# Kernel tuning notes

Measured on AMD Instinct MI355X. Metric: run time of the kernel, lower is better.

## Reference

```python
import jax, jax.numpy as jnp
import numpy as np

INPUT_DIM = 1024
UNITS = 1024

def setup_inputs() -> dict:
    key = jax.random.key(0)
    ks = jax.random.split(key, 7)
    B, S = 4, 2048
    x = jax.random.normal(ks[0], (B, S, INPUT_DIM), dtype=jnp.float32)
    # nn.Linear weights stored as [out, in]; biases [out]
    scale = 1.0 / np.sqrt(INPUT_DIM)
    Wq = jax.random.uniform(ks[1], (UNITS, INPUT_DIM), jnp.float32, -scale, scale)
    bq = jax.random.uniform(ks[2], (UNITS,), jnp.float32, -scale, scale)
    Wk = jax.random.uniform(ks[3], (UNITS, INPUT_DIM), jnp.float32, -scale, scale)
    bk = jax.random.uniform(ks[4], (UNITS,), jnp.float32, -scale, scale)
    Wv = jax.random.uniform(ks[5], (UNITS, INPUT_DIM), jnp.float32, -scale, scale)
    bv = jax.random.uniform(ks[6], (UNITS,), jnp.float32, -scale, scale)
    return {"x": x, "Wq": Wq, "bq": bq, "Wk": Wk, "bk": bk, "Wv": Wv, "bv": bv}

def reference(x, Wq, bq, Wk, bk, Wv, bv):
    # Q/K/V projections: [B,S,D] @ [D,U]
    Q = jnp.einsum('bsd,ud->bsu', x, Wq) + bq
    K = jnp.einsum('bsd,ud->bsu', x, Wk) + bk
    V = jnp.einsum('bsd,ud->bsu', x, Wv) + bv
    scores = jnp.einsum('bqu,bku->bqk', Q, K) / jnp.sqrt(jnp.float32(UNITS))
    attn = jax.nn.softmax(scores, axis=-1)
    return jnp.einsum('bqk,bku->bqu', attn, V)
```

## Files before the change

### kernel.cpp

```cpp
#include <hip/hip_runtime.h>
#include <cstdint>
#include <cstddef>


typedef unsigned short ushort_t;
typedef __attribute__((ext_vector_type(8))) short short8;
typedef __attribute__((ext_vector_type(4))) float f32x4;

#define AS1 __attribute__((address_space(1)))
#define AS3 __attribute__((address_space(3)))

__device__ __forceinline__ ushort_t f2bf(float f) {
    unsigned int u = __float_as_uint(f);
    u += 0x7FFFu + ((u >> 16) & 1u);
    return (ushort_t)(u >> 16);
}
__device__ __forceinline__ float bf2f(ushort_t b) {
    return __uint_as_float(((unsigned)b) << 16);
}

__device__ __forceinline__ void async_ld16(const void* g, unsigned lds_off) {
    __builtin_amdgcn_global_load_lds((const AS1 void*)(uintptr_t)g,
                                     (AS3 void*)(uintptr_t)lds_off,
                                     16, 0, 0);
}

template <typename OT, int EPI, int NB, int BK, int CX, int CY>
__global__ __launch_bounds__(256, 2) void gemm_bt(
    const ushort_t* __restrict__ A, const ushort_t* __restrict__ B0,
    const ushort_t* __restrict__ B1,
    const float* __restrict__ bias0, const float* __restrict__ bias1,
    OT* __restrict__ C0, OT* __restrict__ C1,
    int K, int lda, int ldb, int ldc, float scale,
    long long aOffZ, long long bOffZ, long long cOffZ)
{
    constexpr int P     = BK / 8;
    constexpr int NCALL = BK / 16;
    constexpr int RPC   = 2048 / BK;

    __shared__ __align__(16) ushort_t As[128 * BK];
    __shared__ __align__(16) ushort_t Bs[NB][128 * BK];
    __shared__ float rs[128];

    const int tid  = threadIdx.x;
    const int wave = tid >> 6;
    const int lane = tid & 63;

    const int GX  = gridDim.x, GY = gridDim.y, GZ = gridDim.z;
    const int bid = blockIdx.x + GX * (blockIdx.y + GY * blockIdx.z);
    const int xcd = bid & 7;
    const int jj  = bid >> 3;
    const int CZ  = (GX * GY * GZ) / (8 * CX * CY);
    const int NCX = GX / CX, NCY = GY / CY;
    const int cx  = xcd % NCX;
    const int ct  = xcd / NCX;
    const int cy  = ct % NCY, cz = ct / NCY;
    const int bx  = cx * CX + (jj % CX);
    const int by  = cy * CY + ((jj / CX) % CY);
    const int bz  = cz * CZ + jj / (CX * CY);

    A  += (size_t)bz * aOffZ;
    B0 += (size_t)bz * bOffZ;
    if (NB == 2) B1 += (size_t)bz * bOffZ;

    const int m0 = by * 128;
    const int n0 = bx * 128;
    const int wm = (wave >> 1) * 64;
    const int wn = (wave & 1) * 64;

    const unsigned ldsA  = (unsigned)(uintptr_t)&As[0];
    const unsigned ldsB0 = (unsigned)(uintptr_t)&Bs[0][0];
    const unsigned ldsB1 = (NB == 2) ? (unsigned)(uintptr_t)&Bs[NB - 1][0] : 0;

    const int srow = wave * (RPC / 4) + lane / P;
    const int cd   = ((lane & (P - 1)) - srow) & (P - 1);
    const ushort_t* gA  = A  + (size_t)(m0 + srow) * lda + cd * 8;
    const ushort_t* gB0 = B0 + (size_t)(n0 + srow) * ldb + cd * 8;
    const ushort_t* gB1 = (NB == 2) ? B1 + (size_t)(n0 + srow) * ldb + cd * 8
                                    : nullptr;
    const unsigned lw = (wave << 10);

    const int frow = lane & 15;
    const int fg   = lane >> 4;

    f32x4 acc[NB][4][4] = {};
    float rsacc[4] = {0.f, 0.f, 0.f, 0.f};

    for (int k0 = 0; k0 < K; k0 += BK) {
        if (k0) __syncthreads();
#pragma unroll
        for (int c = 0; c < NCALL; ++c) {
            const size_t ro = (size_t)c * RPC;
            async_ld16(gA + ro * lda, ldsA + c * 4096 + lw);
            async_ld16(gB0 + ro * ldb, ldsB0 + c * 4096 + lw);
            if (NB == 2) async_ld16(gB1 + ro * ldb, ldsB1 + c * 4096 + lw);
        }
        gA += BK; gB0 += BK; if (NB == 2) gB1 += BK;
        __syncthreads();

#pragma unroll
        for (int t = 0; t < BK / 32; ++t) {
            const int pa = (((t << 2) + fg + frow) & (P - 1)) << 3;
            short8 af[4], bf[4];
#pragma unroll
            for (int i = 0; i < 4; ++i)
                af[i] = *(const short8*)&As[(wm + i * 16 + frow) * BK + pa];
            if (EPI == 4 && wn == 0) {
#pragma unroll
                for (int i = 0; i < 4; ++i)
#pragma unroll
                    for (int e = 0; e < 8; ++e)
                        rsacc[i] += bf2f((ushort_t)af[i][e]);
            }
#pragma unroll
            for (int j = 0; j < 4; ++j)
                bf[j] = *(const short8*)&Bs[0][(wn + j * 16 + frow) * BK + pa];
#pragma unroll
            for (int i = 0; i < 4; ++i)
#pragma unroll
                for (int j = 0; j < 4; ++j)
                    acc[0][i][j] = __builtin_amdgcn_mfma_f32_16x16x32_bf16(
                        af[i], bf[j], acc[0][i][j], 0, 0, 0);
            if (NB == 2) {
#pragma unroll
                for (int j = 0; j < 4; ++j)
                    bf[j] = *(const short8*)&Bs[NB - 1][(wn + j * 16 + frow) * BK + pa];
#pragma unroll
                for (int i = 0; i < 4; ++i)
#pragma unroll
                    for (int j = 0; j < 4; ++j)
                        acc[NB - 1][i][j] = __builtin_amdgcn_mfma_f32_16x16x32_bf16(
                            af[i], bf[j], acc[NB - 1][i][j], 0, 0, 0);
            }
        }
    }

    if (EPI == 4) {
        if (wn == 0) {
#pragma unroll
            for (int i = 0; i < 4; ++i) {
                float s = rsacc[i];
                s += __shfl_xor(s, 16, 64);
                s += __shfl_xor(s, 32, 64);
                rs[wm + i * 16 + frow] = s;
            }
        }
        __syncthreads();
    }

    const int r0 = (lane >> 4) << 2;
    const int c0 = lane & 15;
#pragma unroll
    for (int o = 0; o < NB; ++o) {
        OT* C = (o == 0) ? C0 : C1;
        C += (size_t)bz * cOffZ;
        const float* bia = (o == 0) ? bias0 : bias1;
#pragma unroll
        for (int i = 0; i < 4; ++i) {
            float bm[4];
            if (EPI == 2) {
#pragma unroll
                for (int r = 0; r < 4; ++r)
                    bm[r] = bias0[m0 + wm + i * 16 + r0 + r];
            }
            if (EPI == 4) {
#pragma unroll
                for (int r = 0; r < 4; ++r)
                    bm[r] = 1.0f / rs[wm + i * 16 + r0 + r];
            }
#pragma unroll
            for (int j = 0; j < 4; ++j) {
                const int n = n0 + wn + j * 16 + c0;
                const float bn = (EPI == 1) ? bia[n] : 0.f;
#pragma unroll
                for (int r = 0; r < 4; ++r) {
                    const int m = m0 + wm + i * 16 + r0 + r;
                    float v = acc[o][i][j][r] * scale;
                    if (EPI == 1) v += bn;
                    if (EPI == 2) v += bm[r];
                    if (EPI == 3) v = __expf(v);
                    if (EPI == 4) v *= bm[r];
                    if constexpr (sizeof(OT) == 2)
                        C[(size_t)m * ldc + n] = f2bf(v);
                    else
                        C[(size_t)m * ldc + n] = v;
                }
            }
        }
    }
}

__global__ __launch_bounds__(256) void cvt_all(
    const float* __restrict__ x,  const float* __restrict__ wq,
    const float* __restrict__ wk, const float* __restrict__ wv,
    ushort_t* __restrict__ xb,  ushort_t* __restrict__ wqb,
    ushort_t* __restrict__ wkb, ushort_t* __restrict__ wvb)
{
    const int b = blockIdx.x;
    const float* src; ushort_t* dst; size_t base;
    if (b < 4096)      { src = x;  dst = xb;  base = (size_t)b * 2048; }
    else if (b < 4608) { src = wq; dst = wqb; base = (size_t)(b - 4096) * 2048; }
    else if (b < 5120) { src = wk; dst = wkb; base = (size_t)(b - 4608) * 2048; }
    else               { src = wv; dst = wvb; base = (size_t)(b - 5120) * 2048; }
    const size_t i = base + threadIdx.x * 8;
    const f32x4 a = *(const f32x4*)(src + i);
    const f32x4 c = *(const f32x4*)(src + i + 4);
    short8 o;
    o[0] = (short)f2bf(a[0]); o[1] = (short)f2bf(a[1]);
    o[2] = (short)f2bf(a[2]); o[3] = (short)f2bf(a[3]);
    o[4] = (short)f2bf(c[0]); o[5] = (short)f2bf(c[1]);
    o[6] = (short)f2bf(c[2]); o[7] = (short)f2bf(c[3]);
    *(short8*)(dst + i) = o;
}

extern "C" void kernel_launch(void* const* d_in, const int* in_sizes, int n_in,
                              void* d_out, int out_size, void* d_ws, size_t ws_size,
                              hipStream_t stream)
{
    const float* x  = (const float*)d_in[0];
    const float* Wq = (const float*)d_in[1];
    const float* bq = (const float*)d_in[2];
    const float* Wk = (const float*)d_in[3];
    const float* bk = (const float*)d_in[4];
    const float* Wv = (const float*)d_in[5];
    const float* bv = (const float*)d_in[6];
    float* out = (float*)d_out;

    char* ws = (char*)d_ws;
    const size_t MB = 1ull << 20;
    ushort_t* Xb  = (ushort_t*)(ws);
    ushort_t* Wqb = (ushort_t*)(ws + 16 * MB);
    ushort_t* Wkb = (ushort_t*)(ws + 18 * MB);
    ushort_t* Wvb = (ushort_t*)(ws + 20 * MB);
    ushort_t* Qb  = (ushort_t*)(ws + 32 * MB);
    ushort_t* Kb  = (ushort_t*)(ws + 48 * MB);
    ushort_t* Vt  = (ushort_t*)(ws + 64 * MB);
    ushort_t* Sc  = (ushort_t*)(ws);

    cvt_all<<<dim3(5632), dim3(256), 0, stream>>>(
        x, Wq, Wk, Wv, Xb, Wqb, Wkb, Wvb);

    gemm_bt<ushort_t, 1, 2, 64, 4, 16><<<dim3(8, 64, 1), dim3(256), 0, stream>>>(
        Xb, Wqb, Wkb, bq, bk, Qb, Kb, 1024, 1024, 1024, 1024, 1.0f, 0, 0, 0);

    gemm_bt<ushort_t, 2, 1, 64, 16, 4><<<dim3(64, 8, 1), dim3(256), 0, stream>>>(
        Wvb, Xb, nullptr, bv, nullptr, Vt, nullptr,
        1024, 1024, 1024, 8192, 1.0f, 0, 0, 0);

    gemm_bt<ushort_t, 3, 1, 64, 8, 16><<<dim3(16, 16, 4), dim3(256), 0, stream>>>(
        Qb, Kb, nullptr, nullptr, nullptr, Sc, nullptr,
        1024, 1024, 1024, 2048, 0.03125f,
        2048ll * 1024, 2048ll * 1024, 2048ll * 2048);

    gemm_bt<float, 4, 1, 64, 8, 8><<<dim3(8, 16, 4), dim3(256), 0, stream>>>(
        Sc, Vt, nullptr, nullptr, nullptr, out, nullptr,
        2048, 2048, 8192, 1024, 1.0f,
        2048ll * 2048, 2048ll, 2048ll * 1024);
}
```

Baseline: 250.4 us.

## Double-buffer LDS tiles in GEMM and merge Q/K projections into one GEMM

Replaces the single-buffered GEMM, which waited on each tile load before computing, with a double-buffered version that issues async global-to-LDS loads for the next K tile while MFMAs run on the current one. The Q and K projections become one GEMM against the concatenated Wq|Wk weights, producing a single interleaved QK buffer with row stride 2048. The score GEMM then reads Q and K from that buffer with the larger stride. LDS use doubles, which may limit occupancy at two blocks per CU, and the dual-B accumulator path is removed.

```diff
diff --git a/kernel.cpp b/kernel.cpp
--- a/kernel.cpp
+++ b/kernel.cpp
@@ -25,21 +25,19 @@
                                      16, 0, 0);
 }
 
-template <typename OT, int EPI, int NB, int BK, int CX, int CY>
-__global__ __launch_bounds__(256, 2) void gemm_bt(
-    const ushort_t* __restrict__ A, const ushort_t* __restrict__ B0,
-    const ushort_t* __restrict__ B1,
+template <typename OT, int EPI, int CX, int CY>
+__global__ __launch_bounds__(256, 2) void gemm_db(
+    const ushort_t* __restrict__ A, const ushort_t* __restrict__ B,
     const float* __restrict__ bias0, const float* __restrict__ bias1,
-    OT* __restrict__ C0, OT* __restrict__ C1,
-    int K, int lda, int ldb, int ldc, float scale,
+    OT* __restrict__ C, int K, int lda, int ldb, int ldc, float scale,
     long long aOffZ, long long bOffZ, long long cOffZ)
 {
-    constexpr int P     = BK / 8;
-    constexpr int NCALL = BK / 16;
-    constexpr int RPC   = 2048 / BK;
-
-    __shared__ __align__(16) ushort_t As[128 * BK];
-    __shared__ __align__(16) ushort_t Bs[NB][128 * BK];
+    constexpr int BK = 64;
+    constexpr int P  = 8;
+    constexpr int NCALL = 4;
+
+    __shared__ __align__(16) ushort_t As[2][128 * BK];
+    __shared__ __align__(16) ushort_t Bs[2][128 * BK];
     __shared__ float rs[128];
 
     const int tid  = threadIdx.x;
@@ -59,52 +57,57 @@
     const int by  = cy * CY + ((jj / CX) % CY);
     const int bz  = cz * CZ + jj / (CX * CY);
 
-    A  += (size_t)bz * aOffZ;
-    B0 += (size_t)bz * bOffZ;
-    if (NB == 2) B1 += (size_t)bz * bOffZ;
+    A += (size_t)bz * aOffZ;
+    B += (size_t)bz * bOffZ;
 
     const int m0 = by * 128;
     const int n0 = bx * 128;
     const int wm = (wave >> 1) * 64;
     const int wn = (wave & 1) * 64;
 
-    const unsigned ldsA  = (unsigned)(uintptr_t)&As[0];
-    const unsigned ldsB0 = (unsigned)(uintptr_t)&Bs[0][0];
-    const unsigned ldsB1 = (NB == 2) ? (unsigned)(uintptr_t)&Bs[NB - 1][0] : 0;
-
-    const int srow = wave * (RPC / 4) + lane / P;
-    const int cd   = ((lane & (P - 1)) - srow) & (P - 1);
-    const ushort_t* gA  = A  + (size_t)(m0 + srow) * lda + cd * 8;
-    const ushort_t* gB0 = B0 + (size_t)(n0 + srow) * ldb + cd * 8;
-    const ushort_t* gB1 = (NB == 2) ? B1 + (size_t)(n0 + srow) * ldb + cd * 8
-                                    : nullptr;
-    const unsigned lw = (wave << 10);
+    const unsigned aB0 = (unsigned)(uintptr_t)&As[0][0];
+    const unsigned aB1 = (unsigned)(uintptr_t)&As[1][0];
+    const unsigned bB0 = (unsigned)(uintptr_t)&Bs[0][0];
+    const unsigned bB1 = (unsigned)(uintptr_t)&Bs[1][0];
+
+    const int srow = wave * 8 + (lane >> 3);
+    const int cd   = ((lane & 7) - srow) & 7;
+    const unsigned lw = (unsigned)(wave << 10);
+
+    const ushort_t* gA = A + (size_t)(m0 + srow) * lda + cd * 8;
+    const ushort_t* gB = B + (size_t)(n0 + srow) * ldb + cd * 8;
+
+    auto stage = [&](int t) {
+        const int buf = t & 1;
+        const ushort_t* pA = gA + (size_t)t * BK;
+        const ushort_t* pB = gB + (size_t)t * BK;
+        const unsigned la = (buf ? aB1 : aB0) + lw;
+        const unsigned lb = (buf ? bB1 : bB0) + lw;
+#pragma unroll
+        for (int c = 0; c < NCALL; ++c) {
+            async_ld16(pA + (size_t)(c * 32) * lda, la + c * 4096);
+            async_ld16(pB + (size_t)(c * 32) * ldb, lb + c * 4096);
+        }
+    };
 
     const int frow = lane & 15;
     const int fg   = lane >> 4;
 
-    f32x4 acc[NB][4][4] = {};
+    const int NT = K / BK;
+
+    f32x4 acc[4][4] = {};
     float rsacc[4] = {0.f, 0.f, 0.f, 0.f};
 
-    for (int k0 = 0; k0 < K; k0 += BK) {
-        if (k0) __syncthreads();
-#pragma unroll
-        for (int c = 0; c < NCALL; ++c) {
-            const size_t ro = (size_t)c * RPC;
-            async_ld16(gA + ro * lda, ldsA + c * 4096 + lw);
-            async_ld16(gB0 + ro * ldb, ldsB0 + c * 4096 + lw);
-            if (NB == 2) async_ld16(gB1 + ro * ldb, ldsB1 + c * 4096 + lw);
-        }
-        gA += BK; gB0 += BK; if (NB == 2) gB1 += BK;
-        __syncthreads();
-
-#pragma unroll
-        for (int t = 0; t < BK / 32; ++t) {
-            const int pa = (((t << 2) + fg + frow) & (P - 1)) << 3;
+    auto compute = [&](int buf) {
+        const ushort_t* Aw = &As[buf][0];
+        const ushort_t* Bw = &Bs[buf][0];
+#pragma unroll
+        for (int t2 = 0; t2 < 2; ++t2) {
+            const int pa = (((t2 << 2) + fg + frow) & 7) << 3;
             short8 af[4], bf[4];
 #pragma unroll
             for (int i = 0; i < 4; ++i)
-                af[i] = *(const short8*)&As[(wm + i * 16 + frow) * BK + pa];
+                af[i] = *(const short8*)&Aw[(wm + i * 16 + frow) * BK + pa];
             if (EPI == 4 && wn == 0) {
 #pragma unroll
                 for (int i = 0; i < 4; ++i)
@@ -114,26 +117,25 @@
             }
 #pragma unroll
             for (int j = 0; j < 4; ++j)
-                bf[j] = *(const short8*)&Bs[0][(wn + j * 16 + frow) * BK + pa];
+                bf[j] = *(const short8*)&Bw[(wn + j * 16 + frow) * BK + pa];
 #pragma unroll
             for (int i = 0; i < 4; ++i)
 #pragma unroll
                 for (int j = 0; j < 4; ++j)
-                    acc[0][i][j] = __builtin_amdgcn_mfma_f32_16x16x32_bf16(
-                        af[i], bf[j], acc[0][i][j], 0, 0, 0);
-            if (NB == 2) {
-#pragma unroll
-                for (int j = 0; j < 4; ++j)
-                    bf[j] = *(const short8*)&Bs[NB - 1][(wn + j * 16 + frow) * BK + pa];
-#pragma unroll
-                for (int i = 0; i < 4; ++i)
-#pragma unroll
-                    for (int j = 0; j < 4; ++j)
-                        acc[NB - 1][i][j] = __builtin_amdgcn_mfma_f32_16x16x32_bf16(
-                            af[i], bf[j], acc[NB - 1][i][j], 0, 0, 0);
-            }
-        }
+                    acc[i][j] = __builtin_amdgcn_mfma_f32_16x16x32_bf16(
+                        af[i], bf[j], acc[i][j], 0, 0, 0);
+        }
+    };
+
+    stage(0);
+    __syncthreads();
+
+    for (int t = 0; t < NT - 1; ++t) {
+        stage(t + 1);
+        compute(t & 1);
+        __syncthreads();
     }
+    compute((NT - 1) & 1);
 
     if (EPI == 4) {
         if (wn == 0) {
@@ -148,43 +150,39 @@
         __syncthreads();
     }
 
-    const int r0 = (lane >> 4) << 2;
+    C += (size_t)bz * cOffZ;
+    const int r0 = fg << 2;
     const int c0 = lane & 15;
 #pragma unroll
-    for (int o = 0; o < NB; ++o) {
-        OT* C = (o == 0) ? C0 : C1;
-        C += (size_t)bz * cOffZ;
-        const float* bia = (o == 0) ? bias0 : bias1;
-#pragma unroll
-        for (int i = 0; i < 4; ++i) {
-            float bm[4];
-            if (EPI == 2) {
-#pragma unroll
-                for (int r = 0; r < 4; ++r)
-                    bm[r] = bias0[m0 + wm + i * 16 + r0 + r];
-            }
-            if (EPI == 4) {
-#pragma unroll
-                for (int r = 0; r < 4; ++r)
-                    bm[r] = 1.0f / rs[wm + i * 16 + r0 + r];
-            }
-#pragma unroll
-            for (int j = 0; j < 4; ++j) {
-                const int n = n0 + wn + j * 16 + c0;
-                const float bn = (EPI == 1) ? bia[n] : 0.f;
-#pragma unroll
-                for (int r = 0; r < 4; ++r) {
-                    const int m = m0 + wm + i * 16 + r0 + r;
-                    float v = acc[o][i][j][r] * scale;
-                    if (EPI == 1) v += bn;
-                    if (EPI == 2) v += bm[r];
-                    if (EPI == 3) v = __expf(v);
-                    if (EPI == 4) v *= bm[r];
-                    if constexpr (sizeof(OT) == 2)
-                        C[(size_t)m * ldc + n] = f2bf(v);
-                    else
-                        C[(size_t)m * ldc + n] = v;
-                }
+    for (int i = 0; i < 4; ++i) {
+        float bm[4];
+        if (EPI == 2) {
+#pragma unroll
+            for (int r = 0; r < 4; ++r)
+                bm[r] = bias0[m0 + wm + i * 16 + r0 + r];
+        }
+        if (EPI == 4) {
+#pragma unroll
+            for (int r = 0; r < 4; ++r)
+                bm[r] = 1.0f / rs[wm + i * 16 + r0 + r];
+        }
+#pragma unroll
+        for (int j = 0; j < 4; ++j) {
+            const int n = n0 + wn + j * 16 + c0;
+            float bn = 0.f;
+            if (EPI == 1) bn = (n < 1024) ? bias0[n] : bias1[n - 1024];
+#pragma unroll
+            for (int r = 0; r < 4; ++r) {
+                const int m = m0 + wm + i * 16 + r0 + r;
+                float v = acc[i][j][r] * scale;
+                if (EPI == 1) v += bn;
+                if (EPI == 2) v += bm[r];
+                if (EPI == 3) v = __expf(v);
+                if (EPI == 4) v *= bm[r];
+                if constexpr (sizeof(OT) == 2)
+                    C[(size_t)m * ldc + n] = f2bf(v);
+                else
+                    C[(size_t)m * ldc + n] = v;
             }
         }
     }
@@ -228,32 +226,27 @@
 
     char* ws = (char*)d_ws;
     const size_t MB = 1ull << 20;
-    ushort_t* Xb  = (ushort_t*)(ws);
-    ushort_t* Wqb = (ushort_t*)(ws + 16 * MB);
-    ushort_t* Wkb = (ushort_t*)(ws + 18 * MB);
-    ushort_t* Wvb = (ushort_t*)(ws + 20 * MB);
-    ushort_t* Qb  = (ushort_t*)(ws + 32 * MB);
-    ushort_t* Kb  = (ushort_t*)(ws + 48 * MB);
-    ushort_t* Vt  = (ushort_t*)(ws + 64 * MB);
-    ushort_t* Sc  = (ushort_t*)(ws);
+    ushort_t* Xb   = (ushort_t*)(ws);
+    ushort_t* Wqkb = (ushort_t*)(ws + 16 * MB);
+    ushort_t* Wvb  = (ushort_t*)(ws + 20 * MB);
+    ushort_t* QKb  = (ushort_t*)(ws + 32 * MB);
+    ushort_t* Vt   = (ushort_t*)(ws + 64 * MB);
+    ushort_t* Sc   = (ushort_t*)(ws);
 
     cvt_all<<<dim3(5632), dim3(256), 0, stream>>>(
-        x, Wq, Wk, Wv, Xb, Wqb, Wkb, Wvb);
-
-    gemm_bt<ushort_t, 1, 2, 64, 4, 16><<<dim3(8, 64, 1), dim3(256), 0, stream>>>(
-        Xb, Wqb, Wkb, bq, bk, Qb, Kb, 1024, 1024, 1024, 1024, 1.0f, 0, 0, 0);
-
-    gemm_bt<ushort_t, 2, 1, 64, 16, 4><<<dim3(64, 8, 1), dim3(256), 0, stream>>>(
-        Wvb, Xb, nullptr, bv, nullptr, Vt, nullptr,
-        1024, 1024, 1024, 8192, 1.0f, 0, 0, 0);
-
-    gemm_bt<ushort_t, 3, 1, 64, 8, 16><<<dim3(16, 16, 4), dim3(256), 0, stream>>>(
-        Qb, Kb, nullptr, nullptr, nullptr, Sc, nullptr,
-        1024, 1024, 1024, 2048, 0.03125f,
-        2048ll * 1024, 2048ll * 1024, 2048ll * 2048);
-
-    gemm_bt<float, 4, 1, 64, 8, 8><<<dim3(8, 16, 4), dim3(256), 0, stream>>>(
-        Sc, Vt, nullptr, nullptr, nullptr, out, nullptr,
-        2048, 2048, 8192, 1024, 1.0f,
+        x, Wq, Wk, Wv, Xb, Wqkb, (ushort_t*)(ws + 18 * MB), Wvb);
+
+    gemm_db<ushort_t, 1, 8, 16><<<dim3(16, 64, 1), dim3(256), 0, stream>>>(
+        Xb, Wqkb, bq, bk, QKb, 1024, 1024, 1024, 2048, 1.0f, 0, 0, 0);
+
+    gemm_db<ushort_t, 2, 16, 4><<<dim3(64, 8, 1), dim3(256), 0, stream>>>(
+        Wvb, Xb, bv, nullptr, Vt, 1024, 1024, 1024, 8192, 1.0f, 0, 0, 0);
+
+    gemm_db<ushort_t, 3, 8, 16><<<dim3(16, 16, 4), dim3(256), 0, stream>>>(
+        QKb, QKb + 1024, nullptr, nullptr, Sc, 1024, 2048, 2048, 2048,
+        0.03125f, 2048ll * 2048, 2048ll * 2048, 2048ll * 2048);
+
+    gemm_db<float, 4, 8, 8><<<dim3(8, 16, 4), dim3(256), 0, stream>>>(
+        Sc, Vt, nullptr, nullptr, out, 2048, 2048, 8192, 1024, 1.0f,
         2048ll * 2048, 2048ll, 2048ll * 1024);
 }
```

New measurement: 232.2 us. 1.08x faster.
